# Kernel tuning notes

Measured on AMD Instinct MI355X. Metric: run time of the kernel, lower is better.

Reference implementation:

```python
import jax, jax.numpy as jnp
import numpy as np

B, S, D, H = 2, 2048, 1024, 16
EPS = 1e-7  # keras backend epsilon

def setup_inputs() -> dict:
    key = jax.random.key(0)
    ks = jax.random.split(key, 5)
    x = jax.random.normal(ks[0], (B, S, D), dtype=jnp.float32)
    # mem_mask convention: attend where mem_mask == 0 (causal here)
    i = jnp.arange(S)
    causal = (i[None, :] > i[:, None]).astype(jnp.float32)  # 1 = masked
    mem_mask = jnp.broadcast_to(causal[None, None], (B, 1, S, S))
    Wqkv = jax.random.normal(ks[1], (D, 3 * D), dtype=jnp.float32) * (D ** -0.5)
    W_out = jax.random.normal(ks[2], (D, D), dtype=jnp.float32) * (D ** -0.5)
    b_out = jnp.zeros((D,), dtype=jnp.float32)
    scale = jnp.ones((D,), dtype=jnp.float32)
    gate = jax.random.normal(ks[3], (D,), dtype=jnp.float32) * 0.02
    return {"x": x, "mem_mask": mem_mask, "Wqkv": Wqkv, "W_out": W_out,
            "b_out": b_out, "scale": scale, "gate": gate}

def reference(x, mem_mask, Wqkv, W_out, b_out, scale, gate):
    b, s, d = x.shape
    dh = d // H
    h = jnp.einsum('bsd,de->bse', x, Wqkv)
    q, k, v = jnp.split(h, 3, axis=-1)
    def split_heads(t):
        return t.reshape(b, s, H, dh).transpose(0, 2, 1, 3)  # [B,H,S,dh]
    q, k, v = split_heads(q), split_heads(k), split_heads(v)
    q = q * (dh ** -0.5)
    logits = jnp.einsum('bhqd,bhkd->bhqk', q, k)
    logits = logits * (mem_mask == 0.0).astype(logits.dtype)
    weights = jax.nn.relu(logits)
    o = jnp.einsum('bhqk,bhkd->bhqd', weights, v)
    o = o.transpose(0, 2, 1, 3).reshape(b, s, d)  # combine heads
    # Gated RMSNorm
    ms = jnp.mean(o * o, axis=-1, keepdims=True)
    o = scale * o * jax.lax.rsqrt(ms + EPS) * jax.nn.sigmoid(gate * o)
    return jnp.einsum('bsd,de->bse', o, W_out) + b_out
```

## Files before the change

kernel.cpp:

```cpp
#include <hip/hip_runtime.h>
#include <hip/hip_bf16.h>

typedef unsigned short u16;
typedef __attribute__((ext_vector_type(8))) short bf16x8;
typedef __attribute__((ext_vector_type(4))) short short4v;
typedef __attribute__((ext_vector_type(4))) float floatx4;
typedef __attribute__((ext_vector_type(2))) unsigned uint2v;
typedef __attribute__((ext_vector_type(4))) unsigned uint4v;

__device__ __forceinline__ float bf2f(u16 u) {
    unsigned v = ((unsigned)u) << 16;
    return __builtin_bit_cast(float, v);
}
__device__ __forceinline__ u16 f2bf(float f) {
    unsigned u = __builtin_bit_cast(unsigned, f);
    u += 0x7fffu + ((u >> 16) & 1u);
    return (u16)(u >> 16);
}

#define GLDS16(g, l)                                                             \
    __builtin_amdgcn_global_load_lds(                                            \
        (const __attribute__((address_space(1))) void*)(g),                      \
        (__attribute__((address_space(3))) void*)(l), 16, 0, 0)

__device__ __forceinline__ uint2v pl32(unsigned a, unsigned b) {
#if __has_builtin(__builtin_amdgcn_permlane32_swap)
    auto r = __builtin_amdgcn_permlane32_swap(a, b, false, false);
    uint2v o; o.x = (unsigned)r[0]; o.y = (unsigned)r[1]; return o;
#else
    unsigned as = (unsigned)__shfl_xor((int)a, 32, 64);
    unsigned bs = (unsigned)__shfl_xor((int)b, 32, 64);
    const bool hi = (threadIdx.x & 32) != 0;
    uint2v o; o.x = hi ? bs : a; o.y = hi ? b : as; return o;
#endif
}
__device__ __forceinline__ uint2v pl16(unsigned a, unsigned b) {
#if __has_builtin(__builtin_amdgcn_permlane16_swap)
    auto r = __builtin_amdgcn_permlane16_swap(a, b, false, false);
    uint2v o; o.x = (unsigned)r[0]; o.y = (unsigned)r[1]; return o;
#else
    unsigned as = (unsigned)__shfl_xor((int)a, 16, 64);
    unsigned bs = (unsigned)__shfl_xor((int)b, 16, 64);
    const bool odd = (threadIdx.x & 16) != 0;
    uint2v o; o.x = odd ? bs : a; o.y = odd ? b : as; return o;
#endif
}

__global__ __launch_bounds__(256) void prep(const float* __restrict__ x, u16* __restrict__ xb,
                                            const float* __restrict__ Wqkv, u16* __restrict__ WqkvT,
                                            const float* __restrict__ Wout, u16* __restrict__ WoutT) {
    __shared__ u16 t[32][33];
    int blk = blockIdx.x;
    if (blk < 4096) {
        const int i = blk * 256 + threadIdx.x;
        const floatx4 v = ((const floatx4*)x)[i];
        short4v o;
#pragma unroll
        for (int j = 0; j < 4; ++j) o[j] = (short)f2bf(v[j]);
        ((short4v*)xb)[i] = o;
        return;
    }
    const float* in; u16* out; int R, C, bx, by;
    if (blk < 4096 + 3072) { blk -= 4096; in = Wqkv; out = WqkvT; R = 1024; C = 3072; bx = blk % 96; by = blk / 96; }
    else                   { blk -= 7168; in = Wout; out = WoutT; R = 1024; C = 1024; bx = blk & 31; by = blk >> 5; }
    const int c0 = bx * 32, r0 = by * 32;
    const int xx = threadIdx.x & 31, yy = threadIdx.x >> 5;
#pragma unroll
    for (int i = 0; i < 32; i += 8) t[yy + i][xx] = f2bf(in[(size_t)(r0 + yy + i) * C + c0 + xx]);
    __syncthreads();
#pragma unroll
    for (int i = 0; i < 32; i += 8) out[(size_t)(c0 + yy + i) * R + r0 + xx] = t[xx][yy + i];
}

__global__ __launch_bounds__(256, 3) void gemm_qkv(const u16* __restrict__ A, const u16* __restrict__ Bt,
                                                   u16* __restrict__ C, u16* __restrict__ vtp) {
    constexpr int K = 1024, N = 3072;
    __shared__ u16 sA[3][128 * 32];
    __shared__ u16 sB[3][128 * 32];
    const int tid = threadIdx.x;
    const int lane = tid & 63, wave = tid >> 6;
    const int l15 = lane & 15, quad = lane >> 4;
    const int bid = blockIdx.x;
    const int sw = (bid & 7) * 96 + (bid >> 3);
    const int bx = sw % 24, by = sw / 24;
    const int row0 = by * 128, col0 = bx * 128;
    const int wm = (wave & 1) * 64, wn = (wave >> 1) * 64;

    const u16* aq[2]; const u16* bq[2]; int lo[2];
#pragma unroll
    for (int it = 0; it < 2; ++it) {
        const int idx = it * 256 + tid;
        const int r = idx >> 2, bb = idx & 3;
        const int c = bb ^ ((r >> 1) & 3);
        aq[it] = A + (size_t)(row0 + r) * K + c * 8;
        bq[it] = Bt + (size_t)(col0 + r) * K + c * 8;
        lo[it] = idx * 8;
    }
    auto stage = [&](int bufi) {
#pragma unroll
        for (int it = 0; it < 2; ++it) {
            GLDS16(aq[it], &sA[bufi][lo[it]]);
            GLDS16(bq[it], &sB[bufi][lo[it]]);
            aq[it] += 32; bq[it] += 32;
        }
    };

    floatx4 acc[4][4] = {};
    stage(0); stage(1);
    int bc = 0, bn = 1, bs = 2;
    for (int kc = 0; kc < 32; ++kc) {
        if (kc < 31) asm volatile("s_waitcnt vmcnt(4)" ::: "memory");
        else         asm volatile("s_waitcnt vmcnt(0)" ::: "memory");
        __builtin_amdgcn_s_barrier();
        asm volatile("" ::: "memory");
        __builtin_amdgcn_sched_barrier(0);
        if (kc + 2 < 32) stage(bs);

        const u16* sa = sA[bc];
        const u16* sb = sB[bc];
        __builtin_amdgcn_s_setprio(1);
        bf16x8 af[4], bfr[4];
#pragma unroll
        for (int j = 0; j < 4; ++j) {
            const int r = wn + j * 16 + l15;
            const int s = r * 4 + (quad ^ ((r >> 1) & 3));
            bfr[j] = *(const bf16x8*)(sb + s * 8);
        }
#pragma unroll
        for (int i = 0; i < 4; ++i) {
            const int r = wm + i * 16 + l15;
            const int s = r * 4 + (quad ^ ((r >> 1) & 3));
            af[i] = *(const bf16x8*)(sa + s * 8);
        }
#pragma unroll
        for (int i = 0; i < 4; ++i)
#pragma unroll
            for (int j = 0; j < 4; ++j)
                acc[i][j] = __builtin_amdgcn_mfma_f32_16x16x32_bf16(af[i], bfr[j], acc[i][j], 0, 0, 0);
        __builtin_amdgcn_s_setprio(0);
        int t_ = bc; bc = bn; bn = bs; bs = t_;
    }
#pragma unroll
    for (int i = 0; i < 4; ++i) {
#pragma unroll
        for (int j = 0; j < 4; ++j) {
            const int col = col0 + wn + j * 16 + l15;
            const int row = row0 + wm + i * 16 + quad * 4;
#pragma unroll
            for (int r = 0; r < 4; ++r)
                C[(size_t)(row + r) * N + col] = f2bf(acc[i][j][r]);
            if (col0 >= 2048) {
                short4v pk;
#pragma unroll
                for (int r = 0; r < 4; ++r) pk[r] = (short)f2bf(acc[i][j][r] * 0.125f);
                const int bb2 = row >> 11, s = row & 2047;
                const int hd = (col - 2048) >> 6, dh = col & 63;
                *(short4v*)(vtp + ((size_t)(bb2 * 16 + hd) * 64 + dh) * 2048 + s) = pk;
            }
        }
    }
}

__global__ __launch_bounds__(256, 2) void gemm_out(const u16* __restrict__ A, const u16* __restrict__ Bt,
                                                   float* __restrict__ C, const float* __restrict__ bias) {
    constexpr int K = 1024, N = 1024;
    __shared__ u16 sA[3][128 * 32];
    __shared__ u16 sB[3][64 * 32];
    const int tid = threadIdx.x;
    const int lane = tid & 63, wave = tid >> 6;
    const int l15 = lane & 15, quad = lane >> 4;
    const int bid = blockIdx.x;
    const int sw = (bid & 7) * 64 + (bid >> 3);
    const int bx = sw & 15, by = sw >> 4;
    const int row0 = by * 128, col0 = bx * 64;
    const int wm = (wave & 1) * 64, wn = (wave >> 1) * 32;

    const u16* aq[2]; const u16* bq; int lo[2], lob;
#pragma unroll
    for (int it = 0; it < 2; ++it) {
        const int idx = it * 256 + tid;
        const int r = idx >> 2, bb = idx & 3;
        const int c = bb ^ ((r >> 1) & 3);
        aq[it] = A + (size_t)(row0 + r) * K + c * 8;
        lo[it] = idx * 8;
    }
    {
        const int r = tid >> 2, bb = tid & 3;
        const int c = bb ^ ((r >> 1) & 3);
        bq = Bt + (size_t)(col0 + r) * K + c * 8;
        lob = tid * 8;
    }
    auto stage = [&](int bufi) {
        GLDS16(aq[0], &sA[bufi][lo[0]]); aq[0] += 32;
        GLDS16(aq[1], &sA[bufi][lo[1]]); aq[1] += 32;
        GLDS16(bq, &sB[bufi][lob]); bq += 32;
    };

    floatx4 acc[4][2] = {};
    stage(0); stage(1);
    int bc = 0, bn = 1, bs = 2;
    for (int kc = 0; kc < 32; ++kc) {
        if (kc < 31) asm volatile("s_waitcnt vmcnt(3)" ::: "memory");
        else         asm volatile("s_waitcnt vmcnt(0)" ::: "memory");
        __builtin_amdgcn_s_barrier();
        asm volatile("" ::: "memory");
        __builtin_amdgcn_sched_barrier(0);
        if (kc + 2 < 32) stage(bs);

        const u16* sa = sA[bc];
        const u16* sb = sB[bc];
        __builtin_amdgcn_s_setprio(1);
        bf16x8 af[4], bfr[2];
#pragma unroll
        for (int j = 0; j < 2; ++j) {
            const int r = wn + j * 16 + l15;
            const int s = r * 4 + (quad ^ ((r >> 1) & 3));
            bfr[j] = *(const bf16x8*)(sb + s * 8);
        }
#pragma unroll
        for (int i = 0; i < 4; ++i) {
            const int r = wm + i * 16 + l15;
            const int s = r * 4 + (quad ^ ((r >> 1) & 3));
            af[i] = *(const bf16x8*)(sa + s * 8);
        }
#pragma unroll
        for (int i = 0; i < 4; ++i)
#pragma unroll
            for (int j = 0; j < 2; ++j)
                acc[i][j] = __builtin_amdgcn_mfma_f32_16x16x32_bf16(af[i], bfr[j], acc[i][j], 0, 0, 0);
        __builtin_amdgcn_s_setprio(0);
        int t_ = bc; bc = bn; bn = bs; bs = t_;
    }
#pragma unroll
    for (int i = 0; i < 4; ++i) {
#pragma unroll
        for (int j = 0; j < 2; ++j) {
            const int col = col0 + wn + j * 16 + l15;
            const int row = row0 + wm + i * 16 + quad * 4;
            const float b = bias[col];
#pragma unroll
            for (int r = 0; r < 4; ++r)
                C[(size_t)(row + r) * N + col] = acc[i][j][r] + b;
        }
    }
}

__device__ __forceinline__ uint2v pack_relu(floatx4 s, bool diag, int kgb, int qg) {
    float v0 = fmaxf(s[0], 0.f), v1 = fmaxf(s[1], 0.f);
    float v2 = fmaxf(s[2], 0.f), v3 = fmaxf(s[3], 0.f);
    if (diag) {
        if (kgb + 0 > qg) v0 = 0.f;
        if (kgb + 1 > qg) v1 = 0.f;
        if (kgb + 2 > qg) v2 = 0.f;
        if (kgb + 3 > qg) v3 = 0.f;
    }
    uint2v p;
    p.x = ((__builtin_bit_cast(unsigned, v0) + 0x8000u) >> 16) |
          ((__builtin_bit_cast(unsigned, v1) + 0x8000u) & 0xffff0000u);
    p.y = ((__builtin_bit_cast(unsigned, v2) + 0x8000u) >> 16) |
          ((__builtin_bit_cast(unsigned, v3) + 0x8000u) & 0xffff0000u);
    return p;
}

__device__ __forceinline__ bf16x8 pfrag(uint2v A, uint2v B) {
    uint2v gx = pl32(A.x, B.x);
    uint2v dx = pl16(gx.x, gx.y);
    uint2v gy = pl32(A.y, B.y);
    uint2v dy = pl16(gy.x, gy.y);
    uint4v w; w.x = dx.x; w.y = dy.x; w.z = dx.y; w.w = dy.y;
    return __builtin_bit_cast(bf16x8, w);
}

__global__ __launch_bounds__(256, 2) void relu_attn(const u16* __restrict__ h, const u16* __restrict__ vt,
                                                    float* __restrict__ o) {
    union SM {
        struct { u16 K[2][128 * 64]; u16 V[2][64 * 128]; } kv;
        float red[4][64 * 68];
    };
    __shared__ SM sm;
    const int bid = blockIdx.x;
    const int pr = bid >> 5;
    const int bh = bid & 31;
    const int qt64 = 31 - pr;
    const int b = bh >> 4, hd = bh & 15;
    const int tid = threadIdx.x, lane = tid & 63, wave = tid >> 6;
    const int l15 = lane & 15, quad = lane >> 4;
    const int nc = (qt64 >> 1) + 1;

    const int qrow0 = b * 2048 + qt64 * 64;
    bf16x8 qf[4][2];
#pragma unroll
    for (int qt = 0; qt < 4; ++qt)
#pragma unroll
        for (int ks = 0; ks < 2; ++ks)
            qf[qt][ks] = *(const bf16x8*)(h + (size_t)(qrow0 + qt * 16 + l15) * 3072 + hd * 64 + ks * 32 + quad * 8);

    floatx4 acc[4][4] = {};

    const u16* kbase = h + (size_t)(b * 2048) * 3072 + 1024 + hd * 64;
    const u16* vbase = vt + (size_t)bh * 64 * 2048;

    const u16* kq[4]; const u16* vq[4]; int klo[4], vlo[4];
#pragma unroll
    for (int it = 0; it < 4; ++it) {
        const int idx = it * 256 + tid;
        { const int r = idx >> 3, c = idx & 7, cg = c ^ (r & 7);
          kq[it] = kbase + (size_t)r * 3072 + cg * 8; klo[it] = idx * 8; }
        { const int r = idx >> 4, c = idx & 15, cg = c ^ (r & 15);
          vq[it] = vbase + (size_t)r * 2048 + cg * 8; vlo[it] = idx * 8; }
    }
    auto stage = [&](int bufi) {
#pragma unroll
        for (int it = 0; it < 4; ++it) { GLDS16(kq[it], &sm.kv.K[bufi][klo[it]]); kq[it] += 128 * 3072; }
#pragma unroll
        for (int it = 0; it < 4; ++it) { GLDS16(vq[it], &sm.kv.V[bufi][vlo[it]]); vq[it] += 128; }
    };

    stage(0);
    int buf = 0;
    for (int kc = 0; kc < nc; ++kc) {
        asm volatile("s_waitcnt vmcnt(0)" ::: "memory");
        __builtin_amdgcn_s_barrier();
        asm volatile("" ::: "memory");
        __builtin_amdgcn_sched_barrier(0);
        if (kc + 1 < nc) stage(buf ^ 1);

        const u16* sK = sm.kv.K[buf];
        const u16* sV = sm.kv.V[buf];
        __builtin_amdgcn_s_setprio(1);
        bf16x8 kf[2][2];
#pragma unroll
        for (int kt = 0; kt < 2; ++kt)
#pragma unroll
            for (int ks = 0; ks < 2; ++ks) {
                const int row = wave * 32 + kt * 16 + l15;
                const int blk = (quad + ks * 4) ^ (row & 7);
                kf[kt][ks] = *(const bf16x8*)(sK + row * 64 + blk * 8);
            }
        const floatx4 z = {0.f, 0.f, 0.f, 0.f};
        floatx4 s[2][4];
#pragma unroll
        for (int kt = 0; kt < 2; ++kt)
#pragma unroll
            for (int qt = 0; qt < 4; ++qt) {
                floatx4 t = __builtin_amdgcn_mfma_f32_16x16x32_bf16(kf[kt][0], qf[qt][0], z, 0, 0, 0);
                s[kt][qt] = __builtin_amdgcn_mfma_f32_16x16x32_bf16(kf[kt][1], qf[qt][1], t, 0, 0, 0);
            }
        const bool last = (kc == nc - 1);
        uint2v p[2][4];
#pragma unroll
        for (int kt = 0; kt < 2; ++kt)
#pragma unroll
            for (int qt = 0; qt < 4; ++qt)
                p[kt][qt] = pack_relu(s[kt][qt], last,
                                      kc * 128 + wave * 32 + kt * 16 + quad * 4,
                                      qt64 * 64 + qt * 16 + l15);
        bf16x8 vf[4];
#pragma unroll
        for (int nt = 0; nt < 4; ++nt) {
            const int row = nt * 16 + l15;
            const int blk = (wave * 4 + quad) ^ (row & 15);
            vf[nt] = *(const bf16x8*)(sV + row * 128 + blk * 8);
        }
#pragma unroll
        for (int qt = 0; qt < 4; ++qt) {
            const bf16x8 pa = pfrag(p[0][qt], p[1][qt]);
#pragma unroll
            for (int nt = 0; nt < 4; ++nt)
                acc[qt][nt] = __builtin_amdgcn_mfma_f32_16x16x32_bf16(pa, vf[nt], acc[qt][nt], 0, 0, 0);
        }
        __builtin_amdgcn_s_setprio(0);
        buf ^= 1;
    }

    __syncthreads();
    float* rw = sm.red[wave];
#pragma unroll
    for (int qt = 0; qt < 4; ++qt)
#pragma unroll
        for (int nt = 0; nt < 4; ++nt) {
            const int d = nt * 16 + l15, q = qt * 16 + quad * 4;
            *(floatx4*)(rw + d * 68 + q) = acc[qt][nt];
        }
    __syncthreads();
    {
        const int d = lane;
#pragma unroll
        for (int j = 0; j < 4; ++j) {
            const int q = wave * 16 + j * 4;
            floatx4 a = *(const floatx4*)(sm.red[0] + d * 68 + q);
            a += *(const floatx4*)(sm.red[1] + d * 68 + q);
            a += *(const floatx4*)(sm.red[2] + d * 68 + q);
            a += *(const floatx4*)(sm.red[3] + d * 68 + q);
#pragma unroll
            for (int jj = 0; jj < 4; ++jj)
                o[(size_t)(qrow0 + q + jj) * 1024 + hd * 64 + d] = a[jj];
        }
    }
}

__global__ __launch_bounds__(256) void rms_gate(const float* __restrict__ o, const float* __restrict__ scale,
                                                const float* __restrict__ gate, u16* __restrict__ out) {
    const int row = blockIdx.x;
    const int tid = threadIdx.x;
    const floatx4* op = (const floatx4*)(o + (size_t)row * 1024);
    floatx4 v = op[tid];
    float ss = v[0] * v[0] + v[1] * v[1] + v[2] * v[2] + v[3] * v[3];
#pragma unroll
    for (int m = 32; m >= 1; m >>= 1) ss += __shfl_xor(ss, m, 64);
    __shared__ float red[4];
    if ((tid & 63) == 0) red[tid >> 6] = ss;
    __syncthreads();
    const float ms = (red[0] + red[1] + red[2] + red[3]) * (1.0f / 1024.0f);
    const float inv = rsqrtf(ms + 1e-7f);
    const int c = tid * 4;
#pragma unroll
    for (int j = 0; j < 4; ++j) {
        const float s = scale[c + j];
        const float g = gate[c + j];
        const float x = v[j];
        const float sig = 1.0f / (1.0f + __expf(-g * x));
        out[(size_t)row * 1024 + c + j] = f2bf(s * x * inv * sig);
    }
}

extern "C" void kernel_launch(void* const* d_in, const int* in_sizes, int n_in,
                              void* d_out, int out_size, void* d_ws, size_t ws_size,
                              hipStream_t stream) {
    const float* x     = (const float*)d_in[0];
    const float* Wqkv  = (const float*)d_in[2];
    const float* Wout  = (const float*)d_in[3];
    const float* bout  = (const float*)d_in[4];
    const float* scale = (const float*)d_in[5];
    const float* gate  = (const float*)d_in[6];
    float* out = (float*)d_out;

    char* p = (char*)d_ws;
    u16* xb    = (u16*)p; p += (size_t)4096 * 1024 * 2;
    u16* h     = (u16*)p; p += (size_t)4096 * 3072 * 2;
    u16* vt    = (u16*)p; p += (size_t)32 * 64 * 2048 * 2;
    u16* WqkvT = (u16*)p; p += (size_t)3072 * 1024 * 2;
    u16* WoutT = (u16*)p; p += (size_t)1024 * 1024 * 2;
    float* oat = (float*)p; p += (size_t)4096 * 1024 * 4;
    u16* onorm = (u16*)p; p += (size_t)4096 * 1024 * 2;

    prep<<<8192, 256, 0, stream>>>(x, xb, Wqkv, WqkvT, Wout, WoutT);
    gemm_qkv<<<768, 256, 0, stream>>>(xb, WqkvT, h, vt);
    relu_attn<<<1024, 256, 0, stream>>>(h, vt, oat);
    rms_gate<<<4096, 256, 0, stream>>>(oat, scale, gate, onorm);
    gemm_out<<<512, 256, 0, stream>>>(onorm, WoutT, out, bout);
}
```

Before: 197.0 us.

## Single-buffer K/V staging and halve reduction LDS to fit four blocks per CU

Drops double buffering of the K/V tiles in the ReLU attention kernel, so each iteration loads synchronously into a single LDS buffer behind a barrier. It also shrinks the cross-wave reduction scratch from four slabs to two using a two-phase accumulate, and raises launch bounds to four blocks per CU. Both changes cut LDS use so more blocks can be resident, relying on other resident blocks to hide load latency in place of in-block prefetch. The cost is that global-to-LDS loads no longer overlap with MFMA work inside a block, and the tighter register budget under the higher launch bound may cause spills.

Measured after the change: 292.0 us. +48.2%, slower.

```diff
diff --git a/kernel.cpp b/kernel.cpp
--- a/kernel.cpp
+++ b/kernel.cpp
@@ -271,11 +271,11 @@
     return __builtin_bit_cast(bf16x8, w);
 }
 
-__global__ __launch_bounds__(256, 2) void relu_attn(const u16* __restrict__ h, const u16* __restrict__ vt,
+__global__ __launch_bounds__(256, 4) void relu_attn(const u16* __restrict__ h, const u16* __restrict__ vt,
                                                     float* __restrict__ o) {
     union SM {
-        struct { u16 K[2][128 * 64]; u16 V[2][64 * 128]; } kv;
-        float red[4][64 * 68];
+        struct { u16 K[128 * 64]; u16 V[64 * 128]; } kv;
+        float red[2][64 * 68];
     };
     __shared__ SM sm;
     const int bid = blockIdx.x;
@@ -309,24 +309,21 @@
         { const int r = idx >> 4, c = idx & 15, cg = c ^ (r & 15);
           vq[it] = vbase + (size_t)r * 2048 + cg * 8; vlo[it] = idx * 8; }
     }
-    auto stage = [&](int bufi) {
-#pragma unroll
-        for (int it = 0; it < 4; ++it) { GLDS16(kq[it], &sm.kv.K[bufi][klo[it]]); kq[it] += 128 * 3072; }
-#pragma unroll
-        for (int it = 0; it < 4; ++it) { GLDS16(vq[it], &sm.kv.V[bufi][vlo[it]]); vq[it] += 128; }
-    };
-
-    stage(0);
-    int buf = 0;
+
     for (int kc = 0; kc < nc; ++kc) {
+        __builtin_amdgcn_s_barrier();
+        asm volatile("" ::: "memory");
+#pragma unroll
+        for (int it = 0; it < 4; ++it) { GLDS16(kq[it], &sm.kv.K[klo[it]]); kq[it] += 128 * 3072; }
+#pragma unroll
+        for (int it = 0; it < 4; ++it) { GLDS16(vq[it], &sm.kv.V[vlo[it]]); vq[it] += 128; }
         asm volatile("s_waitcnt vmcnt(0)" ::: "memory");
         __builtin_amdgcn_s_barrier();
         asm volatile("" ::: "memory");
         __builtin_amdgcn_sched_barrier(0);
-        if (kc + 1 < nc) stage(buf ^ 1);
-
-        const u16* sK = sm.kv.K[buf];
-        const u16* sV = sm.kv.V[buf];
+
+        const u16* sK = sm.kv.K;
+        const u16* sV = sm.kv.V;
         __builtin_amdgcn_s_setprio(1);
         bf16x8 kf[2][2];
 #pragma unroll
@@ -370,18 +367,32 @@
                 acc[qt][nt] = __builtin_amdgcn_mfma_f32_16x16x32_bf16(pa, vf[nt], acc[qt][nt], 0, 0, 0);
         }
         __builtin_amdgcn_s_setprio(0);
-        buf ^= 1;
     }
 
     __syncthreads();
-    float* rw = sm.red[wave];
-#pragma unroll
-    for (int qt = 0; qt < 4; ++qt)
-#pragma unroll
-        for (int nt = 0; nt < 4; ++nt) {
-            const int d = nt * 16 + l15, q = qt * 16 + quad * 4;
-            *(floatx4*)(rw + d * 68 + q) = acc[qt][nt];
-        }
+    if (wave < 2) {
+        float* rw = sm.red[wave];
+#pragma unroll
+        for (int qt = 0; qt < 4; ++qt)
+#pragma unroll
+            for (int nt = 0; nt < 4; ++nt) {
+                const int d = nt * 16 + l15, q = qt * 16 + quad * 4;
+                *(floatx4*)(rw + d * 68 + q) = acc[qt][nt];
+            }
+    }
+    __syncthreads();
+    if (wave >= 2) {
+        float* rw = sm.red[wave - 2];
+#pragma unroll
+        for (int qt = 0; qt < 4; ++qt)
+#pragma unroll
+            for (int nt = 0; nt < 4; ++nt) {
+                const int d = nt * 16 + l15, q = qt * 16 + quad * 4;
+                floatx4 cur = *(const floatx4*)(rw + d * 68 + q);
+                cur += acc[qt][nt];
+                *(floatx4*)(rw + d * 68 + q) = cur;
+            }
+    }
     __syncthreads();
     {
         const int d = lane;
@@ -390,8 +401,6 @@
             const int q = wave * 16 + j * 4;
             floatx4 a = *(const floatx4*)(sm.red[0] + d * 68 + q);
             a += *(const floatx4*)(sm.red[1] + d * 68 + q);
-            a += *(const floatx4*)(sm.red[2] + d * 68 + q);
-            a += *(const floatx4*)(sm.red[3] + d * 68 + q);
 #pragma unroll
             for (int jj = 0; jj < 4; ++jj)
                 o[(size_t)(qrow0 + q + jj) * 1024 + hd * 64 + d] = a[jj];
```
